# Performance work log

Hardware: AMD Instinct MI355X
Metric: run time of the kernel (lower is better)

## Reference

```python
import jax, jax.numpy as jnp
import numpy as np

N_NODES = 100000
N_EDGES = 1600000
IN_DIM = 128
N_HEADS = 8
OUT_PER_HEAD = 16  # output_dim 128 / 8 heads
LEAKY_SLOPE = 0.2
EPS = 1e-16  # matches PyG softmax denominator epsilon


def setup_inputs() -> dict:
    key = jax.random.key(0)
    k1, k2, k3, k4, k5, k6 = jax.random.split(key, 6)
    x = jax.random.normal(k1, (N_NODES, IN_DIM), dtype=jnp.float32)
    edge_index = jax.random.randint(k2, (2, N_EDGES), 0, N_NODES, dtype=jnp.int32)
    sc = 1.0 / np.sqrt(IN_DIM)
    W_lin = jax.random.normal(k3, (IN_DIM, N_HEADS * OUT_PER_HEAD), dtype=jnp.float32) * sc
    att_l = jax.random.normal(k4, (1, N_HEADS, OUT_PER_HEAD), dtype=jnp.float32) * sc
    att_r = jax.random.normal(k5, (1, N_HEADS, OUT_PER_HEAD), dtype=jnp.float32) * sc
    W_res = jax.random.normal(k6, (IN_DIM, N_HEADS * OUT_PER_HEAD), dtype=jnp.float32) * sc
    return {"x": x, "edge_index": edge_index, "W_lin": W_lin,
            "att_l": att_l, "att_r": att_r, "W_res": W_res}


def reference(x, edge_index, W_lin, att_l, att_r, W_res):
    N = x.shape[0]
    H, C = att_l.shape[1], att_l.shape[2]
    src, dst = edge_index[0], edge_index[1]

    h = (x @ W_lin).reshape(N, H, C)            # [N,H,C]
    alpha_l = (h * att_l).sum(-1)               # [N,H]
    alpha_r = (h * att_r).sum(-1)               # [N,H]

    # per-edge scores, LeakyReLU
    alpha = jax.nn.leaky_relu(alpha_l[src] + alpha_r[dst], LEAKY_SLOPE)  # [E,H]

    # segment softmax grouped by destination node (numerically stable)
    seg_max = jax.ops.segment_max(alpha, dst, num_segments=N)            # [N,H]
    alpha = jnp.exp(alpha - seg_max[dst])
    seg_sum = jax.ops.segment_sum(alpha, dst, num_segments=N)            # [N,H]
    coef = alpha / (seg_sum[dst] + EPS)                                  # [E,H]

    # weighted message scatter-add
    msg = h[src] * coef[:, :, None]                                      # [E,H,C]
    agg = jax.ops.segment_sum(msg, dst, num_segments=N)                  # [N,H,C]

    out = jax.nn.elu(agg).reshape(N, H * C)
    out = out + x @ W_res  # residual
    return out
```

## Files before the change

kernel.cpp:

```cpp
#include <hip/hip_runtime.h>
#include <cstdint>
#include <cstddef>

typedef __attribute__((ext_vector_type(4))) float fvec4;
typedef __attribute__((ext_vector_type(8))) short bf8;
typedef __attribute__((ext_vector_type(8))) unsigned short usvec8;
typedef __attribute__((ext_vector_type(4))) unsigned int uvec4;
typedef __attribute__((ext_vector_type(4))) float f32x4;

#define NNODES 100000
#define NEDGES 1600000
#define INDIM  128
#define HC     128
#define NH     8
#define LEAKY  0.2f
#define SM_EPS 1e-16f
#define BM     64
#define GEMM_BLOCKS ((NNODES + BM - 1) / BM)
#define WROWS  272
#define NBUCK  196
#define NPB_S  512
#define CHUNK  1024
#define CBLK   GEMM_BLOCKS

__device__ __forceinline__ unsigned short f2bf_rne(float f) {
    uint32_t u = __builtin_bit_cast(uint32_t, f);
    u += 0x7FFFu + ((u >> 16) & 1u);
    return (unsigned short)(u >> 16);
}
__device__ __forceinline__ float bf2f(uint32_t lo16) {
    return __builtin_bit_cast(float, lo16 << 16);
}

__global__ __launch_bounds__(256) void k_wt(
    const float* __restrict__ W_lin,
    const float* __restrict__ W_res,
    const float* __restrict__ att_l,
    const float* __restrict__ att_r,
    unsigned short* __restrict__ wt_g)
{
    const int idx = blockIdx.x * 256 + threadIdx.x;
    if (idx >= WROWS * 16) return;
    const int n  = idx >> 4;
    const int k8 = idx & 15;
    usvec8 o;
    if (n < 256) {
        const float* src = (n < 128) ? W_lin : W_res;
        const int col = n & 127;
        #pragma unroll
        for (int j = 0; j < 8; ++j)
            o[j] = f2bf_rne(src[(size_t)(k8 * 8 + j) * HC + col]);
        const int sw = k8 ^ (n & 7);
        *(usvec8*)&wt_g[(size_t)n * INDIM + sw * 8] = o;
    } else {
        const int hd = (n - 256) & 7;
        const float* att = (n < 264) ? att_l : att_r;
        #pragma unroll
        for (int j = 0; j < 8; ++j) {
            const int k = k8 * 8 + j;
            float s = 0.f;
            #pragma unroll
            for (int c = 0; c < 16; ++c)
                s += W_lin[(size_t)k * HC + 16 * hd + c] * att[16 * hd + c];
            o[j] = f2bf_rne(s);
        }
        *(usvec8*)&wt_g[(size_t)n * INDIM + k8 * 8] = o;
    }
}

__global__ __launch_bounds__(256) void k_gemm(
    const float* __restrict__ x,
    const unsigned short* __restrict__ wt_g,
    const int*   __restrict__ ei,
    unsigned short* __restrict__ h16,
    unsigned short* __restrict__ resid16,
    float* __restrict__ alpha_l,
    float* __restrict__ alpha_r,
    int* __restrict__ cnt)
{
    __shared__ unsigned short wt[256 * INDIM];
    __shared__ unsigned short xs[BM * INDIM];

    const int tid = threadIdx.x;
    const size_t nbase = (size_t)blockIdx.x * BM;

    {
        int* hist = (int*)wt;
        if (tid < NBUCK) hist[tid] = 0;
        __syncthreads();
        #pragma unroll
        for (int i = 0; i < CHUNK / 256; ++i) {
            const int e = blockIdx.x * CHUNK + tid + i * 256;
            if (e < NEDGES) atomicAdd(&hist[ei[NEDGES + e] >> 9], 1);
        }
        __syncthreads();
        if (tid < NBUCK) cnt[(size_t)blockIdx.x * NBUCK + tid] = hist[tid];
        __syncthreads();
    }

    {
        const fvec4* s = (const fvec4*)wt_g;
        fvec4* d = (fvec4*)wt;
        #pragma unroll
        for (int i = 0; i < 16; ++i) d[tid + 256 * i] = s[tid + 256 * i];
    }
    {
        const int r0 = tid >> 2;
        const int kq = (tid & 3) * 32;
        const bool valid = (nbase + r0) < NNODES;
        const float* xr = x + (nbase + r0) * INDIM + kq;
        #pragma unroll
        for (int j2 = 0; j2 < 4; ++j2) {
            usvec8 o;
            if (valid) {
                fvec4 p0 = *(const fvec4*)(xr + j2 * 8);
                fvec4 p1 = *(const fvec4*)(xr + j2 * 8 + 4);
                #pragma unroll
                for (int j = 0; j < 4; ++j) { o[j] = f2bf_rne(p0[j]); o[4 + j] = f2bf_rne(p1[j]); }
            } else {
                #pragma unroll
                for (int j = 0; j < 8; ++j) o[j] = 0;
            }
            const int slot = (kq >> 3) + j2;
            const int sw = slot ^ (r0 & 7);
            *(usvec8*)&xs[r0 * INDIM + sw * 8] = o;
        }
    }

    const int wid  = tid >> 6;
    const int lane = tid & 63;
    const int r = lane & 15;
    const int g = lane >> 4;
    const int arow = wid * 16 + r;

    bf8 wa[4];
    #pragma unroll
    for (int kk = 0; kk < 4; ++kk)
        wa[kk] = *(const bf8*)&wt_g[(size_t)(256 + r) * INDIM + kk * 32 + g * 8];

    __syncthreads();

    bf8 a[4];
    #pragma unroll
    for (int kk = 0; kk < 4; ++kk) {
        const int sw = (kk * 4 + g) ^ (arow & 7);
        a[kk] = *(const bf8*)&xs[arow * INDIM + sw * 8];
    }

    f32x4 acc[17];
    #pragma unroll
    for (int t = 0; t < 17; ++t) acc[t] = (f32x4){0.f, 0.f, 0.f, 0.f};

    #pragma unroll
    for (int kk = 0; kk < 4; ++kk) {
        #pragma unroll
        for (int t = 0; t < 16; ++t) {
            const int n = t * 16 + r;
            const int sw = (kk * 4 + g) ^ (n & 7);
            const bf8 b = *(const bf8*)&wt[n * INDIM + sw * 8];
            acc[t] = __builtin_amdgcn_mfma_f32_16x16x32_bf16(a[kk], b, acc[t], 0, 0, 0);
        }
        acc[16] = __builtin_amdgcn_mfma_f32_16x16x32_bf16(a[kk], wa[kk], acc[16], 0, 0, 0);
    }

    #pragma unroll
    for (int ri = 0; ri < 4; ++ri) {
        const size_t node = nbase + wid * 16 + 4 * g + ri;
        if (node < NNODES) {
            if (r < 8) alpha_l[node * NH + r]       = acc[16][ri];
            else       alpha_r[node * NH + (r - 8)] = acc[16][ri];
        }
    }

    __syncthreads();
    unsigned short* st = wt + wid * 4096;
    #pragma unroll
    for (int t = 0; t < 16; ++t) {
        #pragma unroll
        for (int ri = 0; ri < 4; ++ri) {
            const int row = 4 * g + ri;
            st[row * 256 + ((t ^ (row & 7)) << 4) + r] = f2bf_rne(acc[t][ri]);
        }
    }
    __syncthreads();

    {
        const int li = lane & 15;
        const int t  = li >> 1;
        const int half = li & 1;
        #pragma unroll
        for (int it = 0; it < 4; ++it) {
            const int row = it * 4 + (lane >> 4);
            const size_t node = nbase + wid * 16 + row;
            const usvec8 vh = *(const usvec8*)&st[row * 256 + ((t ^ (row & 7)) << 4) + half * 8];
            const usvec8 vr = *(const usvec8*)&st[row * 256 + (((8 + t) ^ (row & 7)) << 4) + half * 8];
            if (node < NNODES) {
                *(usvec8*)&h16[node * HC + li * 8]     = vh;
                *(usvec8*)&resid16[node * HC + li * 8] = vr;
            }
        }
    }
}

__global__ __launch_bounds__(1024) void k_colscan(int* __restrict__ cnt,
                                                  int* __restrict__ btot)
{
    __shared__ int sh[1024];
    const int b = blockIdx.x;
    const int t = threadIdx.x;
    const int i0 = 2 * t, i1 = 2 * t + 1;
    const int v0 = (i0 < CBLK) ? cnt[(size_t)i0 * NBUCK + b] : 0;
    const int v1 = (i1 < CBLK) ? cnt[(size_t)i1 * NBUCK + b] : 0;
    const int s = v0 + v1;
    sh[t] = s;
    __syncthreads();
    #pragma unroll
    for (int off = 1; off < 1024; off <<= 1) {
        int u = (t >= off) ? sh[t - off] : 0;
        __syncthreads();
        sh[t] += u;
        __syncthreads();
    }
    const int base = sh[t] - s;
    if (i0 < CBLK) cnt[(size_t)i0 * NBUCK + b] = base;
    if (i1 < CBLK) cnt[(size_t)i1 * NBUCK + b] = base + v0;
    if (t == 1023) btot[b] = sh[1023];
}

__global__ __launch_bounds__(1024) void k_bscan(const int* __restrict__ btot,
                                                int* __restrict__ bucket_base)
{
    __shared__ int sh[1024];
    const int t = threadIdx.x;
    const int v = (t < NBUCK) ? btot[t] : 0;
    sh[t] = v;
    __syncthreads();
    #pragma unroll
    for (int off = 1; off < 1024; off <<= 1) {
        int u = (t >= off) ? sh[t - off] : 0;
        __syncthreads();
        sh[t] += u;
        __syncthreads();
    }
    if (t < NBUCK) bucket_base[t] = sh[t] - v;
    if (t == 1023) bucket_base[NBUCK] = sh[1023];
}

__global__ __launch_bounds__(256) void k_scat1b(const int* __restrict__ ei,
                                                const int* __restrict__ cnt,
                                                const int* __restrict__ bucket_base,
                                                uint32_t* __restrict__ pairs)
{
    __shared__ int baseabs[NBUCK];
    __shared__ int cur[NBUCK];
    const int t = threadIdx.x;
    if (t < NBUCK) {
        baseabs[t] = cnt[(size_t)blockIdx.x * NBUCK + t] + bucket_base[t];
        cur[t] = 0;
    }
    __syncthreads();
    #pragma unroll
    for (int i = 0; i < CHUNK / 256; ++i) {
        const int e = blockIdx.x * CHUNK + t + i * 256;
        if (e < NEDGES) {
            const int src = ei[e];
            const int dst = ei[NEDGES + e];
            const int b = dst >> 9;
            const int pos = baseabs[b] + atomicAdd(&cur[b], 1);
            pairs[pos] = (uint32_t)src | ((uint32_t)(dst & 511) << 17);
        }
    }
}

__global__ __launch_bounds__(1024) void k_scat2b(const uint32_t* __restrict__ pairs,
                                                 const int* __restrict__ bucket_base,
                                                 int* __restrict__ csr_src,
                                                 int* __restrict__ row_start)
{
    __shared__ int hist[NPB_S];
    __shared__ int rs[NPB_S];
    const int b = blockIdx.x;
    const int t = threadIdx.x;
    const int node_base = b * NPB_S;
    const int nmax = min(NPB_S, NNODES - node_base);

    if (t < NPB_S) hist[t] = 0;
    __syncthreads();

    const int ebeg = bucket_base[b];
    const int eend = bucket_base[b + 1];

    for (int i = ebeg + t; i < eend; i += 1024)
        atomicAdd(&hist[pairs[i] >> 17], 1);
    __syncthreads();

    if (t < NPB_S) rs[t] = hist[t];
    __syncthreads();
    #pragma unroll
    for (int off = 1; off < NPB_S; off <<= 1) {
        int u = (t < NPB_S && t >= off) ? rs[t - off] : 0;
        __syncthreads();
        if (t < NPB_S) rs[t] += u;
        __syncthreads();
    }
    if (t < NPB_S) rs[t] -= hist[t];
    if (t < NPB_S) hist[t] = 0;
    if (t < nmax) row_start[node_base + t] = ebeg + rs[t];
    if (t == 0 && node_base + nmax == NNODES) row_start[NNODES] = eend;
    __syncthreads();

    for (int i = ebeg + t; i < eend; i += 1024) {
        const uint32_t code = pairs[i];
        const int src  = code & 0x1FFFFu;
        const int dstl = code >> 17;
        const int pos = ebeg + rs[dstl] + atomicAdd(&hist[dstl], 1);
        csr_src[pos] = src;
    }
}

__global__ __launch_bounds__(256) void k_msg(
    const int* __restrict__ row_start,
    const int* __restrict__ csr_src,
    const float* __restrict__ alpha_l,
    const float* __restrict__ alpha_r,
    const unsigned short* __restrict__ h16,
    const unsigned short* __restrict__ resid16,
    float* __restrict__ out)
{
    const int n = blockIdx.x * 4 + (threadIdx.x >> 6);
    if (n >= NNODES) return;
    const int lane = threadIdx.x & 63;
    const int sub  = lane >> 3;
    const int li   = lane & 7;

    const int beg = row_start[n];
    const int end = row_start[n + 1];
    const float ar = alpha_r[(size_t)n * NH + li];
    const float* __restrict__ al_li = alpha_l + li;
    const unsigned short* __restrict__ hbase = h16 + 16 * li;

    float ssum = 0.f;
    float acc[16];
    #pragma unroll
    for (int j = 0; j < 16; ++j) acc[j] = 0.f;

    for (int p = beg; p < end; p += 8) {
        const int q = p + sub;
        const bool valid = q < end;
        const int qc = valid ? q : beg;
        const int src = csr_src[qc];
        float a = al_li[(size_t)src * NH] + ar;
        a = a > 0.f ? a : LEAKY * a;
        const float w = valid ? __expf(a) : 0.f;
        ssum += w;
        const unsigned short* hrow = hbase + (size_t)src * HC;
        const uvec4 d0 = *(const uvec4*)hrow;
        const uvec4 d1 = *(const uvec4*)(hrow + 8);
        #pragma unroll
        for (int c = 0; c < 4; ++c) {
            acc[2 * c]         += w * __builtin_bit_cast(float, d0[c] << 16);
            acc[2 * c + 1]     += w * __builtin_bit_cast(float, d0[c] & 0xFFFF0000u);
            acc[8 + 2 * c]     += w * __builtin_bit_cast(float, d1[c] << 16);
            acc[8 + 2 * c + 1] += w * __builtin_bit_cast(float, d1[c] & 0xFFFF0000u);
        }
    }

    ssum += __shfl_xor(ssum, 8);
    ssum += __shfl_xor(ssum, 16);
    ssum += __shfl_xor(ssum, 32);
    #pragma unroll
    for (int j = 0; j < 16; ++j) {
        acc[j] += __shfl_xor(acc[j], 8);
        acc[j] += __shfl_xor(acc[j], 16);
        acc[j] += __shfl_xor(acc[j], 32);
    }

    if (sub == 0) {
        const float inv = 1.f / (ssum + SM_EPS);
        const unsigned short* rrow = resid16 + (size_t)n * HC + 16 * li;
        const uvec4 r0 = *(const uvec4*)rrow;
        const uvec4 r1 = *(const uvec4*)(rrow + 8);
        float res[16];
        #pragma unroll
        for (int c = 0; c < 4; ++c) {
            res[2 * c]         = __builtin_bit_cast(float, r0[c] << 16);
            res[2 * c + 1]     = __builtin_bit_cast(float, r0[c] & 0xFFFF0000u);
            res[8 + 2 * c]     = __builtin_bit_cast(float, r1[c] << 16);
            res[8 + 2 * c + 1] = __builtin_bit_cast(float, r1[c] & 0xFFFF0000u);
        }
        float* orow = out + (size_t)n * HC + 16 * li;
        #pragma unroll
        for (int v4 = 0; v4 < 4; ++v4) {
            fvec4 o;
            #pragma unroll
            for (int j = 0; j < 4; ++j) {
                float v = acc[v4 * 4 + j] * inv;
                o[j] = (v > 0.f ? v : expm1f(v)) + res[v4 * 4 + j];
            }
            *(fvec4*)&orow[v4 * 4] = o;
        }
    }
}

extern "C" void kernel_launch(void* const* d_in, const int* in_sizes, int n_in,
                              void* d_out, int out_size, void* d_ws, size_t ws_size,
                              hipStream_t stream)
{
    const float* x     = (const float*)d_in[0];
    const int*   ei    = (const int*)d_in[1];
    const float* W_lin = (const float*)d_in[2];
    const float* att_l = (const float*)d_in[3];
    const float* att_r = (const float*)d_in[4];
    const float* W_res = (const float*)d_in[5];
    float* out = (float*)d_out;

    unsigned short* wt_g    = (unsigned short*)d_ws;
    unsigned short* h16     = wt_g + (size_t)WROWS * INDIM;
    unsigned short* resid16 = h16 + (size_t)NNODES * HC;
    float* alpha_l  = (float*)(resid16 + (size_t)NNODES * HC);
    float* alpha_r  = alpha_l + (size_t)NNODES * NH;
    int*   cnt      = (int*)(alpha_r + (size_t)NNODES * NH);
    int*   btot     = cnt + (size_t)CBLK * NBUCK;
    int*   bucket_base = btot + NBUCK;
    int*   row_start   = bucket_base + NBUCK + 1;
    uint32_t* pairs = (uint32_t*)(row_start + NNODES + 1);
    int*   csr_src  = (int*)(pairs + NEDGES);

    k_wt<<<17, 256, 0, stream>>>(W_lin, W_res, att_l, att_r, wt_g);
    k_gemm<<<GEMM_BLOCKS, 256, 0, stream>>>(x, wt_g, ei, h16, resid16,
                                            alpha_l, alpha_r, cnt);
    k_colscan<<<NBUCK, 1024, 0, stream>>>(cnt, btot);
    k_bscan<<<1, 1024, 0, stream>>>(btot, bucket_base);
    k_scat1b<<<CBLK, 256, 0, stream>>>(ei, cnt, bucket_base, pairs);
    k_scat2b<<<NBUCK, 1024, 0, stream>>>(pairs, bucket_base, csr_src, row_start);
    k_msg<<<(NNODES + 3) / 4, 256, 0, stream>>>(row_start, csr_src, alpha_l, alpha_r,
                                                h16, resid16, out);
}
```

Measured before the change: 181.0 us.

## Fold bucket scan into scatter kernels and read GEMM weights from global

Removes the single-block k_bscan launch. Each k_scat1b and k_scat2b block now redundantly scans the 196 bucket totals in shared memory. The GEMM kernel no longer stages the 64KB weight tile into LDS; B fragments are read directly from global/L2. The histogram's barriers are overlapped with the x staging. This shrinks LDS per block to raise occupancy and cuts a launch, but adds a redundant scan per block and uncoalesced-ish global B reads inside the MFMA loop.

```diff
diff --git a/kernel.cpp b/kernel.cpp
--- a/kernel.cpp
+++ b/kernel.cpp
@@ -78,32 +78,22 @@
     float* __restrict__ alpha_r,
     int* __restrict__ cnt)
 {
-    __shared__ unsigned short wt[256 * INDIM];
     __shared__ unsigned short xs[BM * INDIM];
+    __shared__ unsigned short st[4 * 16 * 256];
+    __shared__ int hist[NBUCK];
 
     const int tid = threadIdx.x;
     const size_t nbase = (size_t)blockIdx.x * BM;
 
-    {
-        int* hist = (int*)wt;
-        if (tid < NBUCK) hist[tid] = 0;
-        __syncthreads();
-        #pragma unroll
-        for (int i = 0; i < CHUNK / 256; ++i) {
-            const int e = blockIdx.x * CHUNK + tid + i * 256;
-            if (e < NEDGES) atomicAdd(&hist[ei[NEDGES + e] >> 9], 1);
-        }
-        __syncthreads();
-        if (tid < NBUCK) cnt[(size_t)blockIdx.x * NBUCK + tid] = hist[tid];
-        __syncthreads();
-    }
-
-    {
-        const fvec4* s = (const fvec4*)wt_g;
-        fvec4* d = (fvec4*)wt;
-        #pragma unroll
-        for (int i = 0; i < 16; ++i) d[tid + 256 * i] = s[tid + 256 * i];
-    }
+    if (tid < NBUCK) hist[tid] = 0;
+    __syncthreads();
+
+    #pragma unroll
+    for (int i = 0; i < CHUNK / 256; ++i) {
+        const int e = blockIdx.x * CHUNK + tid + i * 256;
+        if (e < NEDGES) atomicAdd(&hist[ei[NEDGES + e] >> 9], 1);
+    }
+
     {
         const int r0 = tid >> 2;
         const int kq = (tid & 3) * 32;
@@ -140,6 +130,8 @@
 
     __syncthreads();
 
+    if (tid < NBUCK) cnt[(size_t)blockIdx.x * NBUCK + tid] = hist[tid];
+
     bf8 a[4];
     #pragma unroll
     for (int kk = 0; kk < 4; ++kk) {
@@ -157,7 +149,7 @@
         for (int t = 0; t < 16; ++t) {
             const int n = t * 16 + r;
             const int sw = (kk * 4 + g) ^ (n & 7);
-            const bf8 b = *(const bf8*)&wt[n * INDIM + sw * 8];
+            const bf8 b = *(const bf8*)&wt_g[(size_t)n * INDIM + sw * 8];
             acc[t] = __builtin_amdgcn_mfma_f32_16x16x32_bf16(a[kk], b, acc[t], 0, 0, 0);
         }
         acc[16] = __builtin_amdgcn_mfma_f32_16x16x32_bf16(a[kk], wa[kk], acc[16], 0, 0, 0);
@@ -172,14 +164,13 @@
         }
     }
 
-    __syncthreads();
-    unsigned short* st = wt + wid * 4096;
+    unsigned short* stw = st + wid * 4096;
     #pragma unroll
     for (int t = 0; t < 16; ++t) {
         #pragma unroll
         for (int ri = 0; ri < 4; ++ri) {
             const int row = 4 * g + ri;
-            st[row * 256 + ((t ^ (row & 7)) << 4) + r] = f2bf_rne(acc[t][ri]);
+            stw[row * 256 + ((t ^ (row & 7)) << 4) + r] = f2bf_rne(acc[t][ri]);
         }
     }
     __syncthreads();
@@ -192,8 +183,8 @@
         for (int it = 0; it < 4; ++it) {
             const int row = it * 4 + (lane >> 4);
             const size_t node = nbase + wid * 16 + row;
-            const usvec8 vh = *(const usvec8*)&st[row * 256 + ((t ^ (row & 7)) << 4) + half * 8];
-            const usvec8 vr = *(const usvec8*)&st[row * 256 + (((8 + t) ^ (row & 7)) << 4) + half * 8];
+            const usvec8 vh = *(const usvec8*)&stw[row * 256 + ((t ^ (row & 7)) << 4) + half * 8];
+            const usvec8 vr = *(const usvec8*)&stw[row * 256 + (((8 + t) ^ (row & 7)) << 4) + half * 8];
             if (node < NNODES) {
                 *(usvec8*)&h16[node * HC + li * 8]     = vh;
                 *(usvec8*)&resid16[node * HC + li * 8] = vr;
@@ -227,35 +218,27 @@
     if (t == 1023) btot[b] = sh[1023];
 }
 
-__global__ __launch_bounds__(1024) void k_bscan(const int* __restrict__ btot,
-                                                int* __restrict__ bucket_base)
-{
-    __shared__ int sh[1024];
-    const int t = threadIdx.x;
-    const int v = (t < NBUCK) ? btot[t] : 0;
-    sh[t] = v;
-    __syncthreads();
-    #pragma unroll
-    for (int off = 1; off < 1024; off <<= 1) {
-        int u = (t >= off) ? sh[t - off] : 0;
-        __syncthreads();
-        sh[t] += u;
-        __syncthreads();
-    }
-    if (t < NBUCK) bucket_base[t] = sh[t] - v;
-    if (t == 1023) bucket_base[NBUCK] = sh[1023];
-}
-
 __global__ __launch_bounds__(256) void k_scat1b(const int* __restrict__ ei,
                                                 const int* __restrict__ cnt,
-                                                const int* __restrict__ bucket_base,
+                                                const int* __restrict__ btot,
                                                 uint32_t* __restrict__ pairs)
 {
+    __shared__ int bb[256];
     __shared__ int baseabs[NBUCK];
     __shared__ int cur[NBUCK];
     const int t = threadIdx.x;
+    const int v = (t < NBUCK) ? btot[t] : 0;
+    bb[t] = v;
+    __syncthreads();
+    #pragma unroll
+    for (int off = 1; off < 256; off <<= 1) {
+        int u = (t >= off) ? bb[t - off] : 0;
+        __syncthreads();
+        bb[t] += u;
+        __syncthreads();
+    }
     if (t < NBUCK) {
-        baseabs[t] = cnt[(size_t)blockIdx.x * NBUCK + t] + bucket_base[t];
+        baseabs[t] = (bb[t] - v) + cnt[(size_t)blockIdx.x * NBUCK + t];
         cur[t] = 0;
     }
     __syncthreads();
@@ -273,22 +256,31 @@
 }
 
 __global__ __launch_bounds__(1024) void k_scat2b(const uint32_t* __restrict__ pairs,
-                                                 const int* __restrict__ bucket_base,
+                                                 const int* __restrict__ btot,
                                                  int* __restrict__ csr_src,
                                                  int* __restrict__ row_start)
 {
     __shared__ int hist[NPB_S];
     __shared__ int rs[NPB_S];
+    __shared__ int bb[256];
     const int b = blockIdx.x;
     const int t = threadIdx.x;
     const int node_base = b * NPB_S;
     const int nmax = min(NPB_S, NNODES - node_base);
 
+    if (t < 256) bb[t] = (t < NBUCK) ? btot[t] : 0;
     if (t < NPB_S) hist[t] = 0;
     __syncthreads();
-
-    const int ebeg = bucket_base[b];
-    const int eend = bucket_base[b + 1];
+    #pragma unroll
+    for (int off = 1; off < 256; off <<= 1) {
+        int u = 0;
+        if (t < 256 && t >= off) u = bb[t - off];
+        __syncthreads();
+        if (t < 256) bb[t] += u;
+        __syncthreads();
+    }
+    const int eend = bb[b];
+    const int ebeg = eend - btot[b];
 
     for (int i = ebeg + t; i < eend; i += 1024)
         atomicAdd(&hist[pairs[i] >> 17], 1);
@@ -421,8 +413,7 @@
     float* alpha_r  = alpha_l + (size_t)NNODES * NH;
     int*   cnt      = (int*)(alpha_r + (size_t)NNODES * NH);
     int*   btot     = cnt + (size_t)CBLK * NBUCK;
-    int*   bucket_base = btot + NBUCK;
-    int*   row_start   = bucket_base + NBUCK + 1;
+    int*   row_start   = btot + NBUCK;
     uint32_t* pairs = (uint32_t*)(row_start + NNODES + 1);
     int*   csr_src  = (int*)(pairs + NEDGES);
 
@@ -430,9 +421,8 @@
     k_gemm<<<GEMM_BLOCKS, 256, 0, stream>>>(x, wt_g, ei, h16, resid16,
                                             alpha_l, alpha_r, cnt);
     k_colscan<<<NBUCK, 1024, 0, stream>>>(cnt, btot);
-    k_bscan<<<1, 1024, 0, stream>>>(btot, bucket_base);
-    k_scat1b<<<CBLK, 256, 0, stream>>>(ei, cnt, bucket_base, pairs);
-    k_scat2b<<<NBUCK, 1024, 0, stream>>>(pairs, bucket_base, csr_src, row_start);
+    k_scat1b<<<CBLK, 256, 0, stream>>>(ei, cnt, btot, pairs);
+    k_scat2b<<<NBUCK, 1024, 0, stream>>>(pairs, btot, csr_src, row_start);
     k_msg<<<(NNODES + 3) / 4, 256, 0, stream>>>(row_start, csr_src, alpha_l, alpha_r,
                                                 h16, resid16, out);
 }
```

Result: slower. 191.5 us (+5.8%).
